# Kernel tuning notes

Measured on AMD Instinct MI355X. Metric: run time of the kernel, lower is better.

Reference implementation:

```python
import jax, jax.numpy as jnp
import numpy as np

N_NODES = 100000
N_EDGES = 1600000
IN_DIM, HID_DIM, OUT_DIM = 128, 128, 40
EPS = 1e-12


def setup_inputs() -> dict:
    key = jax.random.key(0)
    ks = jax.random.split(key, 7)
    x = jax.random.normal(ks[0], (N_NODES, IN_DIM), dtype=jnp.float32)
    edge_index = jax.random.randint(ks[1], (2, N_EDGES), 0, N_NODES, dtype=jnp.int64)
    s1 = 1.0 / np.sqrt(IN_DIM)
    s2 = 1.0 / np.sqrt(HID_DIM)
    return {
        "x": x,
        "edge_index": edge_index,
        "W1_l": jax.random.normal(ks[2], (HID_DIM, IN_DIM), dtype=jnp.float32) * s1,
        "b1": jnp.zeros((HID_DIM,), dtype=jnp.float32),
        "W1_r": jax.random.normal(ks[3], (HID_DIM, IN_DIM), dtype=jnp.float32) * s1,
        "W2_l": jax.random.normal(ks[4], (OUT_DIM, HID_DIM), dtype=jnp.float32) * s2,
        "b2": jnp.zeros((OUT_DIM,), dtype=jnp.float32),
        "W2_r": jax.random.normal(ks[5], (OUT_DIM, HID_DIM), dtype=jnp.float32) * s2,
    }


def _mean_aggregate(x, src, dst, deg_inv):
    # gather source features, scatter-sum into destination nodes, divide by degree
    summed = jax.ops.segment_sum(x[src], dst, num_segments=N_NODES)  # [N, d]
    return summed * deg_inv[:, None]


def _sage_conv(x, src, dst, deg_inv, W_l, b_l, W_r):
    # PyG SAGEConv(mean, normalize=True): lin_l(mean(x_j)) + lin_r(x_i), then L2-normalize
    agg = _mean_aggregate(x, src, dst, deg_inv)
    out = agg @ W_l.T + b_l + x @ W_r.T
    norm = jnp.sqrt(jnp.sum(out * out, axis=-1, keepdims=True))
    return out / jnp.maximum(norm, EPS)


def reference(x, edge_index, W1_l, b1, W1_r, W2_l, b2, W2_r):
    src, dst = edge_index[0], edge_index[1]
    deg = jax.ops.segment_sum(jnp.ones((src.shape[0],), dtype=x.dtype), dst,
                              num_segments=N_NODES)
    deg_inv = 1.0 / jnp.maximum(deg, 1.0)

    h = _sage_conv(x, src, dst, deg_inv, W1_l, b1, W1_r)
    h = jax.nn.relu(h)  # dropout = identity (deterministic reference)
    h = _sage_conv(h, src, dst, deg_inv, W2_l, b2, W2_r)
    h = jax.nn.relu(h)
    return jax.nn.log_softmax(h, axis=-1)
```

## Files before the change

### kernel.cpp

```cpp
#include <hip/hip_runtime.h>
#include <hip/hip_bf16.h>

#define N_NODES 100000
#define N_EDGES 1600000
#define IN_DIM 128
#define HID_DIM 128
#define OUT_DIM 40

#define BSHIFT 9
#define NBUCK 196
#define CHUNK 4096
#define NCHUNK ((N_EDGES + CHUNK - 1) / CHUNK)

typedef __attribute__((ext_vector_type(8))) short short8;
typedef __attribute__((ext_vector_type(4))) float float4v;
typedef __attribute__((ext_vector_type(2))) float f32x2;
typedef __attribute__((ext_vector_type(2))) unsigned int u32x2;
typedef __attribute__((ext_vector_type(4))) unsigned int u32x4;

typedef unsigned char u8;
typedef unsigned short u16;
typedef unsigned int u32;
typedef unsigned long long u64;

__device__ __forceinline__ float bflo(u32 v) { union { u32 u; float f; } c; c.u = v << 16; return c.f; }
__device__ __forceinline__ float bfhi(u32 v) { union { u32 u; float f; } c; c.u = v & 0xffff0000u; return c.f; }
__device__ __forceinline__ u16 f2bf(float f) {
    union { float f; u32 u; } c; c.f = f;
    u32 r = c.u + 0x7fffu + ((c.u >> 16) & 1u);
    return (u16)(r >> 16);
}
__device__ __forceinline__ u32 pk(float lo, float hi) {
    return ((u32)f2bf(hi) << 16) | (u32)f2bf(lo);
}

__device__ __forceinline__ u32 f2fp8(float f) {
    union { float f; u32 u; } c; c.f = f;
    u32 s = (c.u >> 24) & 0x80u;
    u32 a = c.u & 0x7fffffffu;
    u32 code;
    if (a >= 0x3C800000u) {
        if (a > 0x43E00000u) a = 0x43E00000u;
        u32 r = a + 0x0007FFFFu + ((a >> 20) & 1u);
        code = (((r >> 23) - 120u) << 3) | ((r >> 20) & 7u);
        if (code > 0x7Eu) code = 0x7Eu;
    } else {
        union { u32 u; float f; } d; d.u = a;
        code = (u32)(int)rintf(d.f * 512.0f);
    }
    return s | code;
}


#define XBLKS ((N_NODES * IN_DIM / 4 + 255) / 256)
#define WTRIP1 2048
#define WTRIP2 768
#define WBLKS 22

__global__ __launch_bounds__(256) void k_cvtall(
    const float* __restrict__ x, u16* __restrict__ xb, u32* __restrict__ xb8,
    const float* __restrict__ w1l, const float* __restrict__ w1r,
    const float* __restrict__ w2l, const float* __restrict__ w2r,
    u16* __restrict__ w1lf, u16* __restrict__ w1rf,
    u16* __restrict__ w2lf, u16* __restrict__ w2rf,
    const int* __restrict__ idx, int* __restrict__ bucket_size) {
    __shared__ int cnt[NBUCK];
    int b = blockIdx.x;
    if (b < XBLKS) {
        int i = b * 256 + threadIdx.x;
        if (i < N_NODES * IN_DIM / 4) {
            float4v v = reinterpret_cast<const float4v*>(x)[i];
            u32x2 o;
            o.x = pk(v.x, v.y);
            o.y = pk(v.z, v.w);
            reinterpret_cast<u32x2*>(xb)[i] = o;
            u32 r8 = (u32)__builtin_amdgcn_cvt_pk_fp8_f32(v.x, v.y, 0, false);
            r8 = (u32)__builtin_amdgcn_cvt_pk_fp8_f32(v.z, v.w, (int)r8, true);
            xb8[i] = r8;
        }
        return;
    }
    if (b < XBLKS + WBLKS) {
        int i = (b - XBLKS) * 256 + threadIdx.x;
        const float* s; u16* d; int t; int rows;
        if (i < WTRIP1)            { s = w1l; d = w1lf; t = i;                 rows = HID_DIM; }
        else if (i < 2*WTRIP1)     { s = w1r; d = w1rf; t = i - WTRIP1;        rows = HID_DIM; }
        else if (i < 2*WTRIP1+WTRIP2)   { s = w2l; d = w2lf; t = i - 2*WTRIP1; rows = OUT_DIM; }
        else if (i < 2*WTRIP1+2*WTRIP2) { s = w2r; d = w2rf; t = i - 2*WTRIP1-WTRIP2; rows = OUT_DIM; }
        else return;
        int lane = t & 63;
        int ks = (t >> 6) & 3;
        int ct = t >> 8;
        int row = ct * 16 + (lane & 15);
        u32x4 o;
        if (row < rows) {
            const float* sp = s + row * 128;
            if (rows == HID_DIM) {
                int col = ks * 32 + (lane >> 4) * 8;
                float4v v0 = *reinterpret_cast<const float4v*>(sp + col);
                float4v v1 = *reinterpret_cast<const float4v*>(sp + col + 4);
                o.x = pk(v0.x, v0.y); o.y = pk(v0.z, v0.w);
                o.z = pk(v1.x, v1.y); o.w = pk(v1.z, v1.w);
            } else {
                int c0 = ks * 4 + (lane >> 4);
                float f0 = sp[c0];       float f1 = sp[c0 + 16];
                float f2 = sp[c0 + 32];  float f3 = sp[c0 + 48];
                float f4 = sp[c0 + 64];  float f5 = sp[c0 + 80];
                float f6 = sp[c0 + 96];  float f7 = sp[c0 + 112];
                o.x = pk(f0, f1); o.y = pk(f2, f3);
                o.z = pk(f4, f5); o.w = pk(f6, f7);
            }
        } else { o.x = 0; o.y = 0; o.z = 0; o.w = 0; }
        reinterpret_cast<u32x4*>(d)[t] = o;
        return;
    }
    int t = threadIdx.x;
    for (int i = t; i < NBUCK; i += 256) cnt[i] = 0;
    __syncthreads();
    int base = (b - XBLKS - WBLKS) * CHUNK;
    int n = min(CHUNK, N_EDGES - base);
    for (int i = t; i < n; i += 256)
        atomicAdd(&cnt[idx[N_EDGES + base + i] >> BSHIFT], 1);
    __syncthreads();
    for (int i = t; i < NBUCK; i += 256)
        if (cnt[i]) atomicAdd(&bucket_size[i], cnt[i]);
}


__global__ __launch_bounds__(1024) void k_bscatter(const int* __restrict__ idx,
                                                   const int* __restrict__ bucket_size,
                                                   int* __restrict__ bucket_cur,
                                                   u64* __restrict__ rec) {
    __shared__ int cnt[NBUCK], gbase[NBUCK];
    __shared__ int sa[256], sb[256];
    int t = threadIdx.x;
    const int nt = 1024;
    for (int i = t; i < NBUCK; i += nt) cnt[i] = 0;
    __syncthreads();
    int base = blockIdx.x * CHUNK;
    int n = min(CHUNK, N_EDGES - base);
    int eb[4], eq[4];
    u64 er[4];
    #pragma unroll
    for (int k = 0; k < 4; ++k) {
        int i = t + k * nt;
        if (i < n) {
            int srcv = idx[base + i];
            int dstv = idx[N_EDGES + base + i];
            int b = dstv >> BSHIFT;
            eb[k] = b;
            eq[k] = atomicAdd(&cnt[b], 1);
            er[k] = ((u64)(u32)dstv << 32) | (u32)srcv;
        }
    }
    int myv = 0;
    if (t < 256) {
        myv = (t < NBUCK) ? bucket_size[t] : 0;
        sa[t] = myv;
    }
    __syncthreads();
    int *s = sa, *d = sb;
    for (int dd = 1; dd < 256; dd <<= 1) {
        if (t < 256) d[t] = s[t] + ((t >= dd) ? s[t - dd] : 0);
        __syncthreads();
        int* tm = s; s = d; d = tm;
    }
    if (t < NBUCK) {
        int v = cnt[t];
        gbase[t] = v ? (s[t] - myv) + atomicAdd(&bucket_cur[t], v) : 0;
    }
    __syncthreads();
    #pragma unroll
    for (int k = 0; k < 4; ++k) {
        int i = t + k * nt;
        if (i < n) rec[gbase[eb[k]] + eq[k]] = er[k];
    }
}

__global__ __launch_bounds__(1024) void k_bfill(const u64* __restrict__ rec,
                                                const int* __restrict__ bucket_size,
                                                int* __restrict__ row_start,
                                                int* __restrict__ csr) {
    __shared__ int deg[512], cur[512];
    __shared__ int sa[512], sb[512];
    int t = threadIdx.x;
    int nt = blockDim.x;
    int b = blockIdx.x;
    int node0 = b << BSHIFT;
    int nn = min(512, N_NODES - node0);
    int esz = bucket_size[b];
    if (t < 256) sa[t] = (t < NBUCK) ? bucket_size[t] : 0;
    __syncthreads();
    {
        int *s = sa, *d = sb;
        for (int dd = 1; dd < 256; dd <<= 1) {
            if (t < 256) d[t] = s[t] + ((t >= dd) ? s[t - dd] : 0);
            __syncthreads();
            int* tm = s; s = d; d = tm;
        }
        if (t == 0) cur[0] = s[b] - esz;
    }
    __syncthreads();
    int ebase = cur[0];
    __syncthreads();
    for (int i = t; i < 512; i += nt) deg[i] = 0;
    __syncthreads();
    for (int i = t; i < esz; i += nt)
        atomicAdd(&deg[((int)(rec[ebase + i] >> 32)) & 511], 1);
    __syncthreads();
    for (int i = t; i < 512; i += nt) sa[i] = deg[i];
    __syncthreads();
    int *s = sa, *d = sb;
    for (int dd = 1; dd < 512; dd <<= 1) {
        for (int i = t; i < 512; i += nt) d[i] = s[i] + ((i >= dd) ? s[i - dd] : 0);
        __syncthreads();
        int* tm = s; s = d; d = tm;
    }
    for (int i = t; i < 512; i += nt) {
        int excl = s[i] - deg[i];
        cur[i] = excl;
        if (i < nn) row_start[node0 + i] = ebase + excl;
    }
    if (b == NBUCK - 1 && t == 0) row_start[N_NODES] = N_EDGES;
    __syncthreads();
    for (int i = t; i < esz; i += nt) {
        u64 r = rec[ebase + i];
        int dl = ((int)(r >> 32)) & 511;
        int p = atomicAdd(&cur[dl], 1);
        csr[ebase + p] = (int)(r & 0xffffffffu);
    }
}


__global__ void k_agg(const u32x2* __restrict__ fp,
                      const int* __restrict__ csr,
                      const int* __restrict__ row_start,
                      u16* __restrict__ agg) {
    int lane = threadIdx.x & 63;
    int wave = threadIdx.x >> 6;
    int sub = lane >> 4;
    int li = lane & 15;
    int n = blockIdx.x * 16 + wave * 4 + sub;
    int s = row_start[n];
    int e = row_start[n + 1];
    f32x2 ac0 = {0.f, 0.f}, ac1 = {0.f, 0.f}, ac2 = {0.f, 0.f}, ac3 = {0.f, 0.f};
#define ACC8(v) do { \
        ac0 += __builtin_amdgcn_cvt_pk_f32_fp8((v).x, false); \
        ac1 += __builtin_amdgcn_cvt_pk_f32_fp8((v).x, true);  \
        ac2 += __builtin_amdgcn_cvt_pk_f32_fp8((v).y, false); \
        ac3 += __builtin_amdgcn_cvt_pk_f32_fp8((v).y, true);  \
    } while (0)
    int p = s;
    u32x2 v0, v1, v2, v3;
    if (p + 4 <= e) {
        int j0 = csr[p], j1 = csr[p + 1], j2 = csr[p + 2], j3 = csr[p + 3];
        v0 = fp[j0 * 16 + li]; v1 = fp[j1 * 16 + li];
        v2 = fp[j2 * 16 + li]; v3 = fp[j3 * 16 + li];
    }
    while (p + 8 <= e) {
        int k0 = csr[p + 4], k1 = csr[p + 5], k2 = csr[p + 6], k3 = csr[p + 7];
        u32x2 w0 = fp[k0 * 16 + li], w1 = fp[k1 * 16 + li];
        u32x2 w2 = fp[k2 * 16 + li], w3 = fp[k3 * 16 + li];
        ACC8(v0); ACC8(v1); ACC8(v2); ACC8(v3);
        v0 = w0; v1 = w1; v2 = w2; v3 = w3;
        p += 4;
    }
    if (p + 4 <= e) { ACC8(v0); ACC8(v1); ACC8(v2); ACC8(v3); p += 4; }
    while (p < e) { u32x2 v = fp[csr[p] * 16 + li]; ACC8(v); ++p; }
#undef ACC8
    float sc = 1.0f / (float)max(e - s, 1);
    u32x4 o;
    o.x = pk(ac0.x * sc, ac0.y * sc);
    o.y = pk(ac1.x * sc, ac1.y * sc);
    o.z = pk(ac2.x * sc, ac2.y * sc);
    o.w = pk(ac3.x * sc, ac3.y * sc);
    *reinterpret_cast<u32x4*>(agg + n * 128 + li * 8) = o;
}


__global__ __launch_bounds__(256) void k_dense(
    const u16* __restrict__ agg, const u16* __restrict__ x,
    const u16* __restrict__ W1lf, const u16* __restrict__ W1rf,
    const u16* __restrict__ W2lf, const u16* __restrict__ W2rf,
    const float* __restrict__ b1,
    u8* __restrict__ y2, u16* __restrict__ z) {
    __shared__ short8 hbuf[4][4][64];
    int t = threadIdx.x;
    int wave = t >> 6;
    int lane = t & 63;
    int nb = blockIdx.x * 64 + wave * 16;
    int q = lane >> 4;
    int m = lane & 15;
    int arow = nb + m;
    if (arow >= N_NODES) arow = N_NODES - 1;

    short8 afr[8];
    #pragma unroll
    for (int ks = 0; ks < 4; ++ks) {
        afr[ks]     = *reinterpret_cast<const short8*>(agg + arow * 128 + ks * 32 + q * 8);
        afr[4 + ks] = *reinterpret_cast<const short8*>(x   + arow * 128 + ks * 32 + q * 8);
    }
    const short8* g0 = reinterpret_cast<const short8*>(W1lf);
    const short8* g1 = reinterpret_cast<const short8*>(W1rf);

    float4v acc[8];
    #pragma unroll
    for (int ct = 0; ct < 8; ++ct) acc[ct] = (float4v){0.f, 0.f, 0.f, 0.f};

    #pragma unroll
    for (int half = 0; half < 2; ++half) {
        const short8* g = half ? g1 : g0;
        #pragma unroll
        for (int ks = 0; ks < 4; ++ks) {
            short8 a = afr[half * 4 + ks];
            #pragma unroll
            for (int ct = 0; ct < 8; ++ct) {
                short8 bfrag = g[(ct * 4 + ks) * 64 + lane];
                acc[ct] = __builtin_amdgcn_mfma_f32_16x16x32_bf16(a, bfrag, acc[ct], 0, 0, 0);
            }
        }
    }

    float bias[8];
    #pragma unroll
    for (int ct = 0; ct < 8; ++ct) bias[ct] = b1[ct * 16 + m];

    float nsq[4] = { 0.f, 0.f, 0.f, 0.f };
    #pragma unroll
    for (int ct = 0; ct < 8; ++ct)
        #pragma unroll
        for (int r = 0; r < 4; ++r) {
            float v = acc[ct][r] + bias[ct];
            acc[ct][r] = v;
            nsq[r] += v * v;
        }
    #pragma unroll
    for (int r = 0; r < 4; ++r) {
        float tt = nsq[r];
        tt += __shfl_xor(tt, 1);
        tt += __shfl_xor(tt, 2);
        tt += __shfl_xor(tt, 4);
        tt += __shfl_xor(tt, 8);
        nsq[r] = 1.0f / fmaxf(sqrtf(tt), 1e-12f);
    }
    #pragma unroll
    for (int r = 0; r < 4; ++r) {
        short8 hs;
        #pragma unroll
        for (int ct = 0; ct < 8; ++ct)
            hs[ct] = (short)f2bf(fmaxf(acc[ct][r] * nsq[r], 0.0f));
        hbuf[wave][m >> 2][(m & 3) * 16 + q * 4 + r] = hs;
    }

    short8 a2[4];
    #pragma unroll
    for (int ks = 0; ks < 4; ++ks) a2[ks] = hbuf[wave][ks][lane];

    const short8* h0 = reinterpret_cast<const short8*>(W2lf);
    const short8* h1 = reinterpret_cast<const short8*>(W2rf);
    float4v accl[3], accr[3];
    #pragma unroll
    for (int ct = 0; ct < 3; ++ct) {
        accl[ct] = (float4v){0.f, 0.f, 0.f, 0.f};
        accr[ct] = (float4v){0.f, 0.f, 0.f, 0.f};
    }
    #pragma unroll
    for (int ks = 0; ks < 4; ++ks) {
        short8 a = a2[ks];
        #pragma unroll
        for (int ct = 0; ct < 3; ++ct) {
            accl[ct] = __builtin_amdgcn_mfma_f32_16x16x32_bf16(a, h0[(ct * 4 + ks) * 64 + lane], accl[ct], 0, 0, 0);
            accr[ct] = __builtin_amdgcn_mfma_f32_16x16x32_bf16(a, h1[(ct * 4 + ks) * 64 + lane], accr[ct], 0, 0, 0);
        }
    }
    #pragma unroll
    for (int r = 0; r < 4; ++r) {
        int node = nb + q * 4 + r;
        if (node < N_NODES) {
            #pragma unroll
            for (int ct = 0; ct < 3; ++ct) {
                int col = ct * 16 + m;
                y2[node * 64 + col] = (u8)f2fp8(accl[ct][r] * 64.0f);
                z[node * 48 + col]  = f2bf(accr[ct][r]);
            }
            y2[node * 64 + 48 + m] = 0;
        }
    }
}


__global__ void k_agg2(const u32x2* __restrict__ fp,
                       const int* __restrict__ csr,
                       const int* __restrict__ row_start,
                       const u16* __restrict__ z,
                       const float* __restrict__ b2,
                       float* __restrict__ out) {
    int lane = threadIdx.x & 63;
    int wave = threadIdx.x >> 6;
    int sub = lane >> 3;
    int li = lane & 7;
    int n = blockIdx.x * 32 + wave * 8 + sub;
    int s = row_start[n];
    int e = row_start[n + 1];
    f32x2 ac0 = {0.f, 0.f}, ac1 = {0.f, 0.f}, ac2 = {0.f, 0.f}, ac3 = {0.f, 0.f};
#define ACC8(v) do { \
        ac0 += __builtin_amdgcn_cvt_pk_f32_fp8((v).x, false); \
        ac1 += __builtin_amdgcn_cvt_pk_f32_fp8((v).x, true);  \
        ac2 += __builtin_amdgcn_cvt_pk_f32_fp8((v).y, false); \
        ac3 += __builtin_amdgcn_cvt_pk_f32_fp8((v).y, true);  \
    } while (0)
    int p = s;
    u32x2 v0, v1, v2, v3;
    if (p + 4 <= e) {
        int j0 = csr[p], j1 = csr[p + 1], j2 = csr[p + 2], j3 = csr[p + 3];
        v0 = fp[j0 * 8 + li]; v1 = fp[j1 * 8 + li];
        v2 = fp[j2 * 8 + li]; v3 = fp[j3 * 8 + li];
    }
    while (p + 8 <= e) {
        int k0 = csr[p + 4], k1 = csr[p + 5], k2 = csr[p + 6], k3 = csr[p + 7];
        u32x2 w0 = fp[k0 * 8 + li], w1 = fp[k1 * 8 + li];
        u32x2 w2 = fp[k2 * 8 + li], w3 = fp[k3 * 8 + li];
        ACC8(v0); ACC8(v1); ACC8(v2); ACC8(v3);
        v0 = w0; v1 = w1; v2 = w2; v3 = w3;
        p += 4;
    }
    if (p + 4 <= e) { ACC8(v0); ACC8(v1); ACC8(v2); ACC8(v3); p += 4; }
    while (p < e) { u32x2 v = fp[csr[p] * 8 + li]; ACC8(v); ++p; }
#undef ACC8
    float a[8] = { ac0.x, ac0.y, ac1.x, ac1.y, ac2.x, ac2.y, ac3.x, ac3.y };

    float sc = 1.0f / (64.0f * (float)max(e - s, 1));
    float v[8];
    if (li < 5) {
        u32x4 zv = *reinterpret_cast<const u32x4*>(z + n * 48 + li * 8);
        float4v bv0 = *reinterpret_cast<const float4v*>(b2 + li * 8);
        float4v bv1 = *reinterpret_cast<const float4v*>(b2 + li * 8 + 4);
        v[0] = a[0] * sc + bflo(zv.x) + bv0.x;
        v[1] = a[1] * sc + bfhi(zv.x) + bv0.y;
        v[2] = a[2] * sc + bflo(zv.y) + bv0.z;
        v[3] = a[3] * sc + bfhi(zv.y) + bv0.w;
        v[4] = a[4] * sc + bflo(zv.z) + bv1.x;
        v[5] = a[5] * sc + bfhi(zv.z) + bv1.y;
        v[6] = a[6] * sc + bflo(zv.w) + bv1.z;
        v[7] = a[7] * sc + bfhi(zv.w) + bv1.w;
    } else {
        #pragma unroll
        for (int j = 0; j < 8; ++j) v[j] = 0.f;
    }
    float nsq = 0.f;
    #pragma unroll
    for (int j = 0; j < 8; ++j) nsq += v[j] * v[j];
    nsq += __shfl_xor(nsq, 1);
    nsq += __shfl_xor(nsq, 2);
    nsq += __shfl_xor(nsq, 4);
    float rn = 1.0f / fmaxf(sqrtf(nsq), 1e-12f);
    float mv = 0.f;
    #pragma unroll
    for (int j = 0; j < 8; ++j) {
        v[j] = fmaxf(v[j] * rn, 0.f);
        mv = fmaxf(mv, v[j]);
    }
    mv = fmaxf(mv, __shfl_xor(mv, 1));
    mv = fmaxf(mv, __shfl_xor(mv, 2));
    mv = fmaxf(mv, __shfl_xor(mv, 4));
    float se = 0.f;
    if (li < 5) {
        #pragma unroll
        for (int j = 0; j < 8; ++j) se += __expf(v[j] - mv);
    }
    se += __shfl_xor(se, 1);
    se += __shfl_xor(se, 2);
    se += __shfl_xor(se, 4);
    float lse = __logf(se);
    if (li < 5) {
        float4v o0 = { v[0] - mv - lse, v[1] - mv - lse, v[2] - mv - lse, v[3] - mv - lse };
        float4v o1 = { v[4] - mv - lse, v[5] - mv - lse, v[6] - mv - lse, v[7] - mv - lse };
        *reinterpret_cast<float4v*>(out + n * OUT_DIM + li * 8) = o0;
        *reinterpret_cast<float4v*>(out + n * OUT_DIM + li * 8 + 4) = o1;
    }
}


extern "C" void kernel_launch(void* const* d_in, const int* in_sizes, int n_in,
                              void* d_out, int out_size, void* d_ws, size_t ws_size,
                              hipStream_t stream) {
    const float* x   = (const float*)d_in[0];
    const int*   idx = (const int*)d_in[1];
    const float* W1l = (const float*)d_in[2];
    const float* b1  = (const float*)d_in[3];
    const float* W1r = (const float*)d_in[4];
    const float* W2l = (const float*)d_in[5];
    const float* b2  = (const float*)d_in[6];
    const float* W2r = (const float*)d_in[7];
    float* out = (float*)d_out;

    char* ws = (char*)d_ws;
    int*   bucket_size = (int*)(ws + 0);
    int*   bucket_cur  = (int*)(ws + 1024);
    int*   row_start   = (int*)(ws + 16384);
    int*   csr         = (int*)(ws + 1216384);
    u16*   xb          = (u16*)(ws + 7616512);
    u16*   aggb        = (u16*)(ws + 33216512);
    u64*   rec         = (u64*)(ws + 58816512);
    u32*   xb8         = (u32*)(ws + 71616512);
    u8*    y2          = (u8*)(ws + 58816512);
    u16*   z           = (u16*)(ws + 65216512);
    u16*   W1lf        = (u16*)(ws + 84416512);
    u16*   W1rf        = (u16*)(ws + 84449280);
    u16*   W2lf        = (u16*)(ws + 84482048);
    u16*   W2rf        = (u16*)(ws + 84494336);

    hipMemsetAsync(ws, 0, 1808, stream);

    k_cvtall<<<XBLKS + WBLKS + NCHUNK, 256, 0, stream>>>(
        x, xb, xb8, W1l, W1r, W2l, W2r, W1lf, W1rf, W2lf, W2rf, idx, bucket_size);

    k_bscatter<<<NCHUNK, 1024, 0, stream>>>(idx, bucket_size, bucket_cur, rec);
    k_bfill<<<NBUCK, 1024, 0, stream>>>(rec, bucket_size, row_start, csr);

    k_agg<<<N_NODES / 16, 256, 0, stream>>>((const u32x2*)xb8, csr, row_start, aggb);
    k_dense<<<(N_NODES + 63) / 64, 256, 0, stream>>>(aggb, xb, W1lf, W1rf, W2lf, W2rf, b1, y2, z);
    k_agg2<<<N_NODES / 32, 256, 0, stream>>>((const u32x2*)y2, csr, row_start, z, b2, out);
}
```

Measured before the change: 241.0 us.

## Fuse first-layer neighbor aggregation into dense MFMA kernel via LDS

Merges the layer-1 gather/mean kernel into the dense MFMA kernel. Each wave now aggregates its own 16 nodes in four rounds and stores the bf16 results in a swizzled LDS tile, and the MFMA A-fragments are read from LDS instead of a global agg buffer. This removes one kernel launch and the write and re-read of a 25.6 MB bf16 aggregate array. The cost is that the dense kernel now contains the latency-bound gather loop, with fewer nodes in flight per wave (4 per round, serialized) and more LDS use, which may lower occupancy and memory parallelism.

```diff
diff --git a/kernel.cpp b/kernel.cpp
--- a/kernel.cpp
+++ b/kernel.cpp
@@ -232,63 +232,64 @@
 }
 
 
-__global__ void k_agg(const u32x2* __restrict__ fp,
-                      const int* __restrict__ csr,
-                      const int* __restrict__ row_start,
-                      u16* __restrict__ agg) {
-    int lane = threadIdx.x & 63;
-    int wave = threadIdx.x >> 6;
+__global__ __launch_bounds__(256) void k_fused(
+    const u32x2* __restrict__ fp,
+    const int* __restrict__ csr,
+    const int* __restrict__ row_start,
+    const u16* __restrict__ x,
+    const u16* __restrict__ W1lf, const u16* __restrict__ W1rf,
+    const u16* __restrict__ W2lf, const u16* __restrict__ W2rf,
+    const float* __restrict__ b1,
+    u8* __restrict__ y2, u16* __restrict__ z) {
+    __shared__ short8 abuf[4][256];
+    __shared__ short8 hbuf[4][4][64];
+    int t = threadIdx.x;
+    int wave = t >> 6;
+    int lane = t & 63;
+    int nb = blockIdx.x * 64 + wave * 16;
     int sub = lane >> 4;
     int li = lane & 15;
-    int n = blockIdx.x * 16 + wave * 4 + sub;
-    int s = row_start[n];
-    int e = row_start[n + 1];
-    f32x2 ac0 = {0.f, 0.f}, ac1 = {0.f, 0.f}, ac2 = {0.f, 0.f}, ac3 = {0.f, 0.f};
+
+    for (int g4 = 0; g4 < 4; ++g4) {
+        int j = g4 * 4 + sub;
+        int n = nb + j;
+        if (n >= N_NODES) n = N_NODES - 1;
+        int s = row_start[n];
+        int e = row_start[n + 1];
+        f32x2 ac0 = {0.f, 0.f}, ac1 = {0.f, 0.f}, ac2 = {0.f, 0.f}, ac3 = {0.f, 0.f};
 #define ACC8(v) do { \
         ac0 += __builtin_amdgcn_cvt_pk_f32_fp8((v).x, false); \
         ac1 += __builtin_amdgcn_cvt_pk_f32_fp8((v).x, true);  \
         ac2 += __builtin_amdgcn_cvt_pk_f32_fp8((v).y, false); \
         ac3 += __builtin_amdgcn_cvt_pk_f32_fp8((v).y, true);  \
     } while (0)
-    int p = s;
-    u32x2 v0, v1, v2, v3;
-    if (p + 4 <= e) {
-        int j0 = csr[p], j1 = csr[p + 1], j2 = csr[p + 2], j3 = csr[p + 3];
-        v0 = fp[j0 * 16 + li]; v1 = fp[j1 * 16 + li];
-        v2 = fp[j2 * 16 + li]; v3 = fp[j3 * 16 + li];
-    }
-    while (p + 8 <= e) {
-        int k0 = csr[p + 4], k1 = csr[p + 5], k2 = csr[p + 6], k3 = csr[p + 7];
-        u32x2 w0 = fp[k0 * 16 + li], w1 = fp[k1 * 16 + li];
-        u32x2 w2 = fp[k2 * 16 + li], w3 = fp[k3 * 16 + li];
-        ACC8(v0); ACC8(v1); ACC8(v2); ACC8(v3);
-        v0 = w0; v1 = w1; v2 = w2; v3 = w3;
-        p += 4;
-    }
-    if (p + 4 <= e) { ACC8(v0); ACC8(v1); ACC8(v2); ACC8(v3); p += 4; }
-    while (p < e) { u32x2 v = fp[csr[p] * 16 + li]; ACC8(v); ++p; }
+        int p = s;
+        u32x2 v0, v1, v2, v3;
+        if (p + 4 <= e) {
+            int j0 = csr[p], j1 = csr[p + 1], j2 = csr[p + 2], j3 = csr[p + 3];
+            v0 = fp[j0 * 16 + li]; v1 = fp[j1 * 16 + li];
+            v2 = fp[j2 * 16 + li]; v3 = fp[j3 * 16 + li];
+        }
+        while (p + 8 <= e) {
+            int k0 = csr[p + 4], k1 = csr[p + 5], k2 = csr[p + 6], k3 = csr[p + 7];
+            u32x2 w0 = fp[k0 * 16 + li], w1 = fp[k1 * 16 + li];
+            u32x2 w2 = fp[k2 * 16 + li], w3 = fp[k3 * 16 + li];
+            ACC8(v0); ACC8(v1); ACC8(v2); ACC8(v3);
+            v0 = w0; v1 = w1; v2 = w2; v3 = w3;
+            p += 4;
+        }
+        if (p + 4 <= e) { ACC8(v0); ACC8(v1); ACC8(v2); ACC8(v3); p += 4; }
+        while (p < e) { u32x2 v = fp[csr[p] * 16 + li]; ACC8(v); ++p; }
 #undef ACC8
-    float sc = 1.0f / (float)max(e - s, 1);
-    u32x4 o;
-    o.x = pk(ac0.x * sc, ac0.y * sc);
-    o.y = pk(ac1.x * sc, ac1.y * sc);
-    o.z = pk(ac2.x * sc, ac2.y * sc);
-    o.w = pk(ac3.x * sc, ac3.y * sc);
-    *reinterpret_cast<u32x4*>(agg + n * 128 + li * 8) = o;
-}
-
-
-__global__ __launch_bounds__(256) void k_dense(
-    const u16* __restrict__ agg, const u16* __restrict__ x,
-    const u16* __restrict__ W1lf, const u16* __restrict__ W1rf,
-    const u16* __restrict__ W2lf, const u16* __restrict__ W2rf,
-    const float* __restrict__ b1,
-    u8* __restrict__ y2, u16* __restrict__ z) {
-    __shared__ short8 hbuf[4][4][64];
-    int t = threadIdx.x;
-    int wave = t >> 6;
-    int lane = t & 63;
-    int nb = blockIdx.x * 64 + wave * 16;
+        float sc = 1.0f / (float)max(e - s, 1);
+        union { u32x4 u; short8 s8; } o;
+        o.u.x = pk(ac0.x * sc, ac0.y * sc);
+        o.u.y = pk(ac1.x * sc, ac1.y * sc);
+        o.u.z = pk(ac2.x * sc, ac2.y * sc);
+        o.u.w = pk(ac3.x * sc, ac3.y * sc);
+        abuf[wave][j * 16 + (li ^ (j & 7))] = o.s8;
+    }
+
     int q = lane >> 4;
     int m = lane & 15;
     int arow = nb + m;
@@ -297,8 +298,8 @@
     short8 afr[8];
     #pragma unroll
     for (int ks = 0; ks < 4; ++ks) {
-        afr[ks]     = *reinterpret_cast<const short8*>(agg + arow * 128 + ks * 32 + q * 8);
-        afr[4 + ks] = *reinterpret_cast<const short8*>(x   + arow * 128 + ks * 32 + q * 8);
+        afr[ks]     = abuf[wave][m * 16 + ((4 * ks + q) ^ (m & 7))];
+        afr[4 + ks] = *reinterpret_cast<const short8*>(x + arow * 128 + ks * 32 + q * 8);
     }
     const short8* g0 = reinterpret_cast<const short8*>(W1lf);
     const short8* g1 = reinterpret_cast<const short8*>(W1rf);
@@ -500,11 +501,10 @@
     int*   row_start   = (int*)(ws + 16384);
     int*   csr         = (int*)(ws + 1216384);
     u16*   xb          = (u16*)(ws + 7616512);
-    u16*   aggb        = (u16*)(ws + 33216512);
+    u8*    y2          = (u8*)(ws + 33216512);
+    u16*   z           = (u16*)(ws + 39616512);
     u64*   rec         = (u64*)(ws + 58816512);
     u32*   xb8         = (u32*)(ws + 71616512);
-    u8*    y2          = (u8*)(ws + 58816512);
-    u16*   z           = (u16*)(ws + 65216512);
     u16*   W1lf        = (u16*)(ws + 84416512);
     u16*   W1rf        = (u16*)(ws + 84449280);
     u16*   W2lf        = (u16*)(ws + 84482048);
@@ -518,7 +518,7 @@
     k_bscatter<<<NCHUNK, 1024, 0, stream>>>(idx, bucket_size, bucket_cur, rec);
     k_bfill<<<NBUCK, 1024, 0, stream>>>(rec, bucket_size, row_start, csr);
 
-    k_agg<<<N_NODES / 16, 256, 0, stream>>>((const u32x2*)xb8, csr, row_start, aggb);
-    k_dense<<<(N_NODES + 63) / 64, 256, 0, stream>>>(aggb, xb, W1lf, W1rf, W2lf, W2rf, b1, y2, z);
+    k_fused<<<(N_NODES + 63) / 64, 256, 0, stream>>>(
+        (const u32x2*)xb8, csr, row_start, xb, W1lf, W1rf, W2lf, W2rf, b1, y2, z);
     k_agg2<<<N_NODES / 32, 256, 0, stream>>>((const u32x2*)y2, csr, row_start, z, b2, out);
 }
```

Measured after the change: 258.4 us. 7.2% more time.
